# Kernel optimization log

Hardware: AMD Instinct MI355X
Metric: run time of the kernel (lower is better)

Reference implementation:

```python
import jax, jax.numpy as jnp
import numpy as np

D = 2048      # hidden_size
H = 16        # heads
HD = D // H   # head_dim = 128
FF = 8192     # intermediate_size
B = 4
S = 2048
FACTOR = 0.5  # mod_router_factor
EPS = 1e-6


def setup_inputs() -> dict:
    key = jax.random.key(0)
    ks = jax.random.split(key, 10)
    w = lambda k, shape: jax.random.normal(k, shape, jnp.float32) * 0.02
    return {
        "hidden_states": jax.random.normal(ks[0], (B, S, D), jnp.float32),
        "position_ids": jnp.arange(S, dtype=jnp.int32)[None, :],
        "mod_target_mask": jnp.ones((B, S), dtype=bool),
        "attention_mask_2d": jnp.ones((B, S), dtype=bool),
        "router_w": w(ks[1], (D,)),
        "ln1_w": jnp.ones((D,), jnp.float32),
        "ln2_w": jnp.ones((D,), jnp.float32),
        "Wq": w(ks[2], (D, D)),
        "Wk": w(ks[3], (D, D)),
        "Wv": w(ks[4], (D, D)),
        "Wo": w(ks[5], (D, D)),
        "W1": w(ks[6], (D, FF)),
        "W2": w(ks[7], (FF, D)),
    }


def _rmsnorm(x, w):
    return x * jax.lax.rsqrt(jnp.mean(x * x, axis=-1, keepdims=True) + EPS) * w


def _rope(x, pos):
    # x: [B,K,H,HD], pos: [B,K]
    half = HD // 2
    freqs = 1.0 / (10000.0 ** (jnp.arange(half, dtype=jnp.float32) / half))
    ang = pos[:, :, None].astype(jnp.float32) * freqs  # [B,K,half]
    cos = jnp.cos(ang)[:, :, None, :]
    sin = jnp.sin(ang)[:, :, None, :]
    x1, x2 = x[..., :half], x[..., half:]
    return jnp.concatenate([x1 * cos - x2 * sin, x2 * cos + x1 * sin], axis=-1)


def reference(hidden_states, position_ids, mod_target_mask, attention_mask_2d,
              router_w, ln1_w, ln2_w, Wq, Wk, Wv, Wo, W1, W2):
    Bq, Sq, _ = hidden_states.shape
    K = int(Sq * FACTOR)  # static top-k length (all rows fully mod-targeted)

    # --- token router ---
    logits = jnp.einsum('bsd,d->bs', hidden_states, router_w)
    logits = jnp.where(mod_target_mask, logits, -jnp.inf)
    weights = jax.nn.sigmoid(logits)  # weight_normalization: sigmoid * 1.0 + 0.0

    # --- top-k dispatch (indices sorted to preserve sequence order, matching
    # torch boolean-mask gather of kept tokens) ---
    _, idx = jax.lax.top_k(weights, K)
    idx = jnp.sort(idx, axis=1)                       # [B,K]
    bidx = jnp.arange(Bq)[:, None]
    kept = hidden_states[bidx, idx]                   # [B,K,D] residual
    pos = jnp.broadcast_to(position_ids, (Bq, Sq))[bidx, idx]

    # --- decoder layer (Llama-style pre-norm block) on kept tokens ---
    h1 = _rmsnorm(kept, ln1_w)
    q = _rope((h1 @ Wq).reshape(Bq, K, H, HD), pos)
    k = _rope((h1 @ Wk).reshape(Bq, K, H, HD), pos)
    v = (h1 @ Wv).reshape(Bq, K, H, HD)
    scores = jnp.einsum('bqhd,bkhd->bhqk', q, k) / np.sqrt(HD).astype(np.float32)
    causal = jnp.tril(jnp.ones((K, K), dtype=bool))
    scores = jnp.where(causal, scores, jnp.finfo(scores.dtype).min)
    attn = jax.nn.softmax(scores, axis=-1)
    ao = jnp.einsum('bhqk,bkhd->bqhd', attn, v).reshape(Bq, K, D) @ Wo
    h2 = kept + ao
    mlp = jax.nn.gelu(_rmsnorm(h2, ln2_w) @ W1) @ W2
    delta = ao + mlp  # forward_return_residual: layer_out - residual

    # --- combine: hidden[kept]=delta; hidden[target]*=w; hidden[kept]+=residual ---
    out = hidden_states.at[bidx, idx].set(delta)
    out = jnp.where(mod_target_mask[..., None], out * weights[..., None], out)
    out = out.at[bidx, idx].add(kept)
    return out
```

## Files before the change

### kernel.cpp

```cpp
#include <hip/hip_runtime.h>
#include <stdint.h>

#define Dm 2048
#define Hn 16
#define HDm 128
#define FFm 8192
#define Bm 4
#define Sm 2048
#define Km 1024

typedef __attribute__((ext_vector_type(4))) float f32x4;
typedef __attribute__((ext_vector_type(8))) short s16x8;
typedef unsigned short u16;
typedef unsigned int u32;

__device__ __forceinline__ float bf_lo(u32 u){ u32 x = u << 16; return __builtin_bit_cast(float, x); }
__device__ __forceinline__ float bf_hi(u32 u){ u32 x = u & 0xffff0000u; return __builtin_bit_cast(float, x); }
__device__ __forceinline__ float bfu(u16 u){ u32 x = ((u32)u) << 16; return __builtin_bit_cast(float, x); }
__device__ __forceinline__ u16 f2bf(float f){
  u32 u = __builtin_bit_cast(u32, f);
  u += 0x7fffu + ((u >> 16) & 1u);
  return (u16)(u >> 16);
}
__device__ __forceinline__ u32 pack2(float a, float b){
  return (u32)f2bf(a) | ((u32)f2bf(b) << 16);
}
__device__ __forceinline__ void unpack8(uint4 a, float* f){
  f[0]=bf_lo(a.x); f[1]=bf_hi(a.x); f[2]=bf_lo(a.y); f[3]=bf_hi(a.y);
  f[4]=bf_lo(a.z); f[5]=bf_hi(a.z); f[6]=bf_lo(a.w); f[7]=bf_hi(a.w);
}
__device__ __forceinline__ uint4 pack8(const float* f){
  uint4 o; o.x=pack2(f[0],f[1]); o.y=pack2(f[2],f[3]); o.z=pack2(f[4],f[5]); o.w=pack2(f[6],f[7]); return o;
}
__device__ __forceinline__ void load8_in(const void* p, size_t off, int fp32, float* f){
  if (fp32){
    const float* pf = (const float*)p + off;
    float4 a = *(const float4*)pf;
    float4 b = *(const float4*)(pf + 4);
    f[0]=a.x; f[1]=a.y; f[2]=a.z; f[3]=a.w;
    f[4]=b.x; f[5]=b.y; f[6]=b.z; f[7]=b.w;
  } else {
    uint4 a = *(const uint4*)((const u16*)p + off);
    unpack8(a, f);
  }
}
__device__ __forceinline__ float gelu_f(float x){
  float t = tanhf(0.7978845608028654f*(x + 0.044715f*x*x*x));
  return 0.5f*x*(1.0f + t);
}
__device__ __forceinline__ float block_sum256(float s){
  #pragma unroll
  for (int off = 32; off; off >>= 1) s += __shfl_xor(s, off);
  __shared__ float red[4];
  int lane = threadIdx.x & 63, w = threadIdx.x >> 6;
  if (lane == 0) red[w] = s;
  __syncthreads();
  return red[0] + red[1] + red[2] + red[3];
}
__device__ __forceinline__ void gload_lds16(const u16* g, u16* l){
  __builtin_amdgcn_global_load_lds((const __attribute__((address_space(1))) void*)g,
                                   (__attribute__((address_space(3))) void*)l, 16, 0, 0);
}

__global__ __launch_bounds__(256) void sniff_kernel(const u32* __restrict__ hs, int* __restrict__ flag){
  __shared__ int s;
  if (threadIdx.x == 0) s = 0;
  __syncthreads();
  int bad = 0;
  for (int i = threadIdx.x; i < 4096; i += 256){
    u32 w = hs[i];
    float lo = bf_lo(w), hi = bf_hi(w);
    if (!(fabsf(lo) < 1000.f && fabsf(hi) < 1000.f)) bad = 1;
  }
  if (bad) atomicOr(&s, 1);
  __syncthreads();
  if (threadIdx.x == 0) flag[0] = s;
}

__global__ __launch_bounds__(256) void router_kernel(const void* __restrict__ hs, const void* __restrict__ rw,
                                                     const int* __restrict__ dflag,
                                                     float* __restrict__ weights, int* __restrict__ selmap){
  int fp32 = *dflag;
  int row = blockIdx.x, t = threadIdx.x;
  float a[8], b8[8];
  load8_in(hs, (size_t)row*Dm + t*8, fp32, a);
  load8_in(rw, (size_t)t*8, fp32, b8);
  float s = 0.f;
  #pragma unroll
  for (int i = 0; i < 8; i++) s += a[i]*b8[i];
  float tot = block_sum256(s);
  if (t == 0){
    weights[row] = 1.0f/(1.0f + expf(-tot));
    selmap[row] = -1;
  }
}

__global__ __launch_bounds__(1024) void topk_kernel(const float* __restrict__ weights, const int* __restrict__ position_ids,
                                                    int* __restrict__ idx, int* __restrict__ pos, int* __restrict__ selmap){
  int b = blockIdx.x, t = threadIdx.x;
  __shared__ float v[Sm];
  __shared__ int id[Sm];
  v[t] = weights[b*Sm + t];             id[t] = t;
  v[t+1024] = weights[b*Sm + t + 1024]; id[t+1024] = t + 1024;
  for (int size = 2; size <= Sm; size <<= 1){
    for (int stride = size >> 1; stride > 0; stride >>= 1){
      __syncthreads();
      int lo = ((t & ~(stride-1)) << 1) | (t & (stride-1));
      int hi = lo + stride;
      bool up = (lo & size) == 0;
      float va = v[lo], vb = v[hi]; int ia = id[lo], ib = id[hi];
      bool aFirst = (va > vb) || (va == vb && ia < ib);
      if (up ? !aFirst : aFirst){ v[lo]=vb; v[hi]=va; id[lo]=ib; id[hi]=ia; }
    }
  }
  __syncthreads();
  for (int size = 2; size <= Km; size <<= 1){
    for (int stride = size >> 1; stride > 0; stride >>= 1){
      __syncthreads();
      if (t < Km/2){
        int lo = ((t & ~(stride-1)) << 1) | (t & (stride-1));
        int hi = lo + stride;
        bool up = (lo & size) == 0;
        int ia = id[lo], ib = id[hi];
        bool aFirst = ia < ib;
        if (up ? !aFirst : aFirst){ id[lo]=ib; id[hi]=ia; }
      }
    }
  }
  __syncthreads();
  if (t < Km){
    int iv = id[t];
    idx[b*Km + t] = iv;
    pos[b*Km + t] = position_ids[iv];
    selmap[b*Sm + iv] = t;
  }
}

__global__ __launch_bounds__(256) void gather_rmsnorm(const void* __restrict__ hs, const int* __restrict__ idx,
                                                      const void* __restrict__ ln1, const int* __restrict__ dflag,
                                                      u16* __restrict__ h1){
  int fp32 = *dflag;
  int g = blockIdx.x, t = threadIdx.x;
  int b = g >> 10;
  int row = idx[g];
  float f[8];
  load8_in(hs, ((size_t)b*Sm + row)*Dm + t*8, fp32, f);
  float ss = 0.f;
  #pragma unroll
  for (int i = 0; i < 8; i++) ss += f[i]*f[i];
  float tot = block_sum256(ss);
  float scale = rsqrtf(tot * (1.0f/Dm) + 1e-6f);
  float lw[8];
  load8_in(ln1, (size_t)t*8, fp32, lw);
  float o[8];
  #pragma unroll
  for (int i = 0; i < 8; i++) o[i] = f[i]*scale*lw[i];
  ((uint4*)(h1 + (size_t)g*Dm))[t] = pack8(o);
}

__global__ __launch_bounds__(256) void h2norm_kernel(const void* __restrict__ hs, const int* __restrict__ idx,
                                                     const u16* __restrict__ ao, const void* __restrict__ ln2,
                                                     const int* __restrict__ dflag, u16* __restrict__ h2n){
  int fp32 = *dflag;
  int g = blockIdx.x, t = threadIdx.x;
  int b = g >> 10;
  int row = idx[g];
  float ke[8], av[8];
  load8_in(hs, ((size_t)b*Sm + row)*Dm + t*8, fp32, ke);
  unpack8(((const uint4*)(ao + (size_t)g*Dm))[t], av);
  float f[8]; float ss = 0.f;
  #pragma unroll
  for (int i = 0; i < 8; i++){ f[i] = ke[i] + av[i]; ss += f[i]*f[i]; }
  float tot = block_sum256(ss);
  float scale = rsqrtf(tot * (1.0f/Dm) + 1e-6f);
  float lw[8];
  load8_in(ln2, (size_t)t*8, fp32, lw);
  float o[8];
  #pragma unroll
  for (int i = 0; i < 8; i++) o[i] = f[i]*scale*lw[i];
  ((uint4*)(h2n + (size_t)g*Dm))[t] = pack8(o);
}

__global__ __launch_bounds__(256) void transpose_k(const void* __restrict__ src, const int* __restrict__ dflag,
                                                   u16* __restrict__ dst, int R, int C, int ldS, size_t srcOff){
  int fp32 = *dflag;
  __shared__ u16 tile[64][72];
  int c0 = blockIdx.x << 6, r0 = blockIdx.y << 6;
  int t = threadIdx.x;
  int rr = t >> 3, cc = (t & 7) * 8;
  #pragma unroll
  for (int p = 0; p < 2; p++){
    float f[8];
    load8_in(src, srcOff + (size_t)(r0 + rr + p*32) * ldS + c0 + cc, fp32, f);
    u16 tmp[8];
    #pragma unroll
    for (int j = 0; j < 8; j++) tmp[j] = f2bf(f[j]);
    *(uint4*)&tile[rr + p*32][cc] = *(const uint4*)tmp;
  }
  __syncthreads();
  int col = t >> 3, r8 = (t & 7) * 8;
  #pragma unroll
  for (int p = 0; p < 2; p++){
    u16 tmp[8];
    #pragma unroll
    for (int j = 0; j < 8; j++) tmp[j] = tile[r8 + j][col + p*32];
    *(uint4*)(dst + (size_t)(c0 + col + p*32) * R + r0 + r8) = *(const uint4*)tmp;
  }
}

__global__ __launch_bounds__(256) void transpose_v(const u16* __restrict__ src, u16* __restrict__ dst){
  __shared__ u16 tile[64][72];
  int bh = blockIdx.z; int b = bh >> 4, h = bh & 15;
  int key0 = blockIdx.x << 6;
  int d0 = blockIdx.y << 6;
  int t = threadIdx.x;
  int rr = t >> 3, cc = (t & 7) * 8;
  #pragma unroll
  for (int p = 0; p < 2; p++){
    uint4 a = *(const uint4*)(src + ((size_t)(b*Km + key0 + rr + p*32))*Dm + h*HDm + d0 + cc);
    *(uint4*)&tile[rr + p*32][cc] = a;
  }
  __syncthreads();
  int col = t >> 3, r8 = (t & 7) * 8;
  #pragma unroll
  for (int p = 0; p < 2; p++){
    u16 tmp[8];
    #pragma unroll
    for (int j = 0; j < 8; j++) tmp[j] = tile[r8 + j][col + p*32];
    *(uint4*)(dst + ((size_t)bh*HDm + d0 + col + p*32)*Km + key0 + r8) = *(const uint4*)tmp;
  }
}

template<int BN>
__global__ __launch_bounds__(512, 2) void gemm256(const u16* __restrict__ A, const u16* __restrict__ BT,
                                                  u16* __restrict__ Cmat, int Kd, int lda, int ldb, int ldc,
                                                  int do_gelu, int accum){
  extern __shared__ u16 lds[];
  constexpr int WC    = BN / 4;
  constexpr int NREP  = BN / 64;
  constexpr int BTILE = BN * 64;
  constexpr int BROWS = BN / 8;
  constexpr int NSTGB = BN / 64;
  const int t    = threadIdx.x;
  const int lane = t & 63, wid = t >> 6;
  const int wr = wid >> 2, wc = wid & 3;
  const int l16 = lane & 15, quad = lane >> 4;
  const int m0 = blockIdx.x * 256, n0 = blockIdx.y * BN;

  const int lrow = lane >> 3;
  const int csw  = (lane & 7) ^ lrow;
  const u16* gA = A  + (size_t)(m0 + wid*32    + lrow) * lda + csw*8;
  const u16* gB = BT + (size_t)(n0 + wid*BROWS + lrow) * ldb + csw*8;

  f32x4 acc[8][NREP];
  #pragma unroll
  for (int i = 0; i < 8; i++)
    #pragma unroll
    for (int j = 0; j < NREP; j++) acc[i][j] = (f32x4){0.f,0.f,0.f,0.f};

  auto STAGE = [&](int buf, int kt){
    u16* la = lds + buf*16384 + (wid*32)*64;
    #pragma unroll
    for (int s = 0; s < 4; s++)
      gload_lds16(gA + (size_t)(s*8)*lda + kt*64, la + (s*8)*64);
    u16* lb = lds + 32768 + buf*BTILE + (wid*BROWS)*64;
    #pragma unroll
    for (int s = 0; s < NSTGB; s++)
      gload_lds16(gB + (size_t)(s*8)*ldb + kt*64, lb + (s*8)*64);
  };

  const int NT = Kd >> 6;
  STAGE(0, 0);
  for (int kt = 0; kt < NT; kt++){
    const int cur = kt & 1;
    if (kt + 1 < NT){
      STAGE(cur ^ 1, kt + 1);
      if constexpr (BN == 256) asm volatile("s_waitcnt vmcnt(8)" ::: "memory");
      else                     asm volatile("s_waitcnt vmcnt(6)" ::: "memory");
    } else {
      asm volatile("s_waitcnt vmcnt(0)" ::: "memory");
    }
    __builtin_amdgcn_s_barrier();
    __builtin_amdgcn_sched_barrier(0);
    const u16* LA = lds + cur*16384;
    const u16* LB = lds + 32768 + cur*BTILE;
    const int rsw = l16 & 7;
    s16x8 bf[NREP][2];
    #pragma unroll
    for (int ni = 0; ni < NREP; ni++)
      #pragma unroll
      for (int ks = 0; ks < 2; ks++)
        bf[ni][ks] = *(const s16x8*)(LB + (wc*WC + ni*16 + l16)*64 + ((ks*4 + quad) ^ rsw)*8);
    #pragma unroll
    for (int mi = 0; mi < 8; mi++){
      const u16* ar = LA + (wr*128 + mi*16 + l16)*64;
      s16x8 a0 = *(const s16x8*)(ar + ((quad     ^ rsw)*8));
      s16x8 a1 = *(const s16x8*)(ar + (((4+quad) ^ rsw)*8));
      __builtin_amdgcn_s_setprio(1);
      #pragma unroll
      for (int ni = 0; ni < NREP; ni++){
        acc[mi][ni] = __builtin_amdgcn_mfma_f32_16x16x32_bf16(a0, bf[ni][0], acc[mi][ni], 0, 0, 0);
        acc[mi][ni] = __builtin_amdgcn_mfma_f32_16x16x32_bf16(a1, bf[ni][1], acc[mi][ni], 0, 0, 0);
      }
      __builtin_amdgcn_s_setprio(0);
    }
    asm volatile("" ::: "memory");
    __builtin_amdgcn_s_barrier();
    __builtin_amdgcn_sched_barrier(0);
  }

  if (accum){
    __syncthreads();
    float* Cf = (float*)lds;
    #pragma unroll
    for (int mi = 0; mi < 8; mi++)
      #pragma unroll
      for (int ni = 0; ni < NREP; ni++){
        int rb = wr*128 + mi*16 + quad*4;
        int col = wc*WC + ni*16 + l16;
        #pragma unroll
        for (int r = 0; r < 4; r++) Cf[(rb + r)*BN + col] = acc[mi][ni][r];
      }
    __syncthreads();
    constexpr int CH = (256*BN)/4096;
    #pragma unroll
    for (int i = 0; i < CH; i++){
      int off = i*4096 + t*8;
      int row = off / BN, col = off % BN;
      u16* cp = Cmat + (size_t)(m0 + row)*ldc + n0 + col;
      uint4 old = *(const uint4*)cp;
      float f[8]; unpack8(old, f);
      float4 a = *(const float4*)(Cf + off);
      float4 b2 = *(const float4*)(Cf + off + 4);
      float o[8] = {a.x+f[0], a.y+f[1], a.z+f[2], a.w+f[3],
                    b2.x+f[4], b2.y+f[5], b2.z+f[6], b2.w+f[7]};
      *(uint4*)cp = pack8(o);
    }
  } else {
    __syncthreads();
    u16* Ct = lds;
    #pragma unroll
    for (int mi = 0; mi < 8; mi++)
      #pragma unroll
      for (int ni = 0; ni < NREP; ni++){
        int rb = wr*128 + mi*16 + quad*4;
        int col = wc*WC + ni*16 + l16;
        #pragma unroll
        for (int r = 0; r < 4; r++){
          float v = acc[mi][ni][r];
          if (do_gelu) v = gelu_f(v);
          Ct[(rb + r)*BN + col] = f2bf(v);
        }
      }
    __syncthreads();
    constexpr int CH = (256*BN)/4096;
    #pragma unroll
    for (int i = 0; i < CH; i++){
      int off = i*4096 + t*8;
      int row = off / BN, col = off % BN;
      uint4 v = *(const uint4*)(Ct + off);
      *(uint4*)(Cmat + (size_t)(m0 + row)*ldc + n0 + col) = v;
    }
  }
}

__global__ __launch_bounds__(256) void rope_kernel(u16* __restrict__ qkb, const int* __restrict__ pos){
  int tid = blockIdx.x*256 + threadIdx.x;
  int row = tid >> 6, d = tid & 63;
  int grow = row >> 4, h = row & 15;
  float p = (float)pos[grow];
  float freq = exp2f(-0.20762050593589063f * (float)d);
  float ang = p * freq;
  float cs = cosf(ang), sn = sinf(ang);
  size_t base = (size_t)grow * 4096 + h*HDm + d;
  float x1 = bfu(qkb[base]), x2 = bfu(qkb[base+64]);
  qkb[base]    = f2bf(x1*cs - x2*sn);
  qkb[base+64] = f2bf(x2*cs + x1*sn);
  x1 = bfu(qkb[base+2048]); x2 = bfu(qkb[base+2048+64]);
  qkb[base+2048]    = f2bf(x1*cs - x2*sn);
  qkb[base+2048+64] = f2bf(x2*cs + x1*sn);
}

__global__ __launch_bounds__(256) void attn_mfma(const u16* __restrict__ qk, const u16* __restrict__ vt,
                                                 u16* __restrict__ o){
  __shared__ __align__(16) u16 Plds[4][32][72];
  const int w = threadIdx.x >> 6;
  const int lane = threadIdx.x & 63;
  const int l16 = lane & 15, quad = lane >> 4;
  const int bh = blockIdx.y;
  const int b = bh >> 4, h = bh & 15;
  const int bxr = (int)gridDim.x - 1 - (int)blockIdx.x;
  const int q0 = bxr * 128 + w * 32;
  const int QLD = 4096;

  s16x8 aq[2][4];
  #pragma unroll
  for (int qt = 0; qt < 2; qt++){
    const u16* qrow = qk + ((size_t)b*Km + q0 + qt*16 + l16)*QLD + h*HDm;
    #pragma unroll
    for (int kk = 0; kk < 4; kk++) aq[qt][kk] = *(const s16x8*)(qrow + kk*32 + quad*8);
  }
  const u16* kbase = qk + (size_t)b*Km*QLD + 2048 + h*HDm;
  const u16* vth   = vt + (size_t)bh * HDm * Km;

  f32x4 accO[2][8];
  #pragma unroll
  for (int qt = 0; qt < 2; qt++)
    #pragma unroll
    for (int n = 0; n < 8; n++) accO[qt][n] = (f32x4){0.f,0.f,0.f,0.f};
  float mrow[2][4], lrow[2][4];
  #pragma unroll
  for (int qt = 0; qt < 2; qt++)
    #pragma unroll
    for (int r = 0; r < 4; r++){ mrow[qt][r] = -1e30f; lrow[qt][r] = 0.f; }

  const float c = 0.08838834764831845f * 1.4426950408889634f;
  const int qmax = q0 + 31;

  for (int kt = 0; kt <= qmax; kt += 64){
    float sv[4][2][4];
    #pragma unroll
    for (int half = 0; half < 4; half++){
      s16x8 bk[4];
      const u16* krow = kbase + (size_t)(kt + half*16 + l16)*QLD;
      #pragma unroll
      for (int kk = 0; kk < 4; kk++) bk[kk] = *(const s16x8*)(krow + kk*32 + quad*8);
      int key = kt + half*16 + l16;
      #pragma unroll
      for (int qt = 0; qt < 2; qt++){
        f32x4 s = (f32x4){0.f,0.f,0.f,0.f};
        #pragma unroll
        for (int kk = 0; kk < 4; kk++)
          s = __builtin_amdgcn_mfma_f32_16x16x32_bf16(aq[qt][kk], bk[kk], s, 0, 0, 0);
        #pragma unroll
        for (int r = 0; r < 4; r++)
          sv[half][qt][r] = (key <= q0 + qt*16 + quad*4 + r) ? s[r]*c : -1e30f;
      }
    }
    float alpha[2][4];
    #pragma unroll
    for (int qt = 0; qt < 2; qt++){
      #pragma unroll
      for (int r = 0; r < 4; r++){
        float cm = fmaxf(fmaxf(sv[0][qt][r], sv[1][qt][r]), fmaxf(sv[2][qt][r], sv[3][qt][r]));
        cm = fmaxf(cm, __shfl_xor(cm, 1));
        cm = fmaxf(cm, __shfl_xor(cm, 2));
        cm = fmaxf(cm, __shfl_xor(cm, 4));
        cm = fmaxf(cm, __shfl_xor(cm, 8));
        float mn = fmaxf(mrow[qt][r], cm);
        alpha[qt][r] = __builtin_amdgcn_exp2f(mrow[qt][r] - mn);
        mrow[qt][r] = mn;
        float ps = 0.f;
        #pragma unroll
        for (int hh = 0; hh < 4; hh++){
          float p = __builtin_amdgcn_exp2f(sv[hh][qt][r] - mn);
          u16 u = f2bf(p);
          Plds[w][qt*16 + quad*4 + r][hh*16 + l16] = u;
          ps += bfu(u);
        }
        ps += __shfl_xor(ps, 1);
        ps += __shfl_xor(ps, 2);
        ps += __shfl_xor(ps, 4);
        ps += __shfl_xor(ps, 8);
        lrow[qt][r] = lrow[qt][r]*alpha[qt][r] + ps;
      }
    }
    asm volatile("s_waitcnt lgkmcnt(0)" ::: "memory");
    __builtin_amdgcn_sched_barrier(0);
    s16x8 ap[2][2];
    #pragma unroll
    for (int qt = 0; qt < 2; qt++){
      ap[qt][0] = *(const s16x8*)&Plds[w][qt*16 + l16][quad*8];
      ap[qt][1] = *(const s16x8*)&Plds[w][qt*16 + l16][32 + quad*8];
    }
    #pragma unroll
    for (int qt = 0; qt < 2; qt++)
      #pragma unroll
      for (int n = 0; n < 8; n++)
        #pragma unroll
        for (int r = 0; r < 4; r++) accO[qt][n][r] *= alpha[qt][r];
    #pragma unroll
    for (int n = 0; n < 8; n++){
      const u16* vrow = vth + (size_t)(n*16 + l16)*Km + kt;
      s16x8 bv0 = *(const s16x8*)(vrow + quad*8);
      s16x8 bv1 = *(const s16x8*)(vrow + 32 + quad*8);
      accO[0][n] = __builtin_amdgcn_mfma_f32_16x16x32_bf16(ap[0][0], bv0, accO[0][n], 0, 0, 0);
      accO[0][n] = __builtin_amdgcn_mfma_f32_16x16x32_bf16(ap[0][1], bv1, accO[0][n], 0, 0, 0);
      accO[1][n] = __builtin_amdgcn_mfma_f32_16x16x32_bf16(ap[1][0], bv0, accO[1][n], 0, 0, 0);
      accO[1][n] = __builtin_amdgcn_mfma_f32_16x16x32_bf16(ap[1][1], bv1, accO[1][n], 0, 0, 0);
    }
  }

  #pragma unroll
  for (int qt = 0; qt < 2; qt++){
    float inv[4];
    #pragma unroll
    for (int r = 0; r < 4; r++) inv[r] = 1.0f / lrow[qt][r];
    #pragma unroll
    for (int n = 0; n < 8; n++)
      #pragma unroll
      for (int r = 0; r < 4; r++){
        size_t off = ((size_t)b*Km + q0 + qt*16 + quad*4 + r)*Dm + h*HDm + n*16 + l16;
        o[off] = f2bf(accO[qt][n][r]*inv[r]);
      }
  }
}

__global__ __launch_bounds__(256) void final_kernel(const void* __restrict__ hidden, const float* __restrict__ weights,
                                                    const int* __restrict__ selmap, const u16* __restrict__ delta,
                                                    const int* __restrict__ dflag, void* __restrict__ outv){
  int fp32 = *dflag;
  int row = blockIdx.x, t = threadIdx.x;
  int b = row >> 11;
  float w = weights[row];
  int sel = selmap[row];
  float hv[8];
  load8_in(hidden, (size_t)row*Dm + t*8, fp32, hv);
  float f[8];
  if (sel >= 0){
    size_t ko = ((size_t)(b*Km + sel))*Dm;
    float dv[8];
    unpack8(((const uint4*)(delta+ko))[t], dv);
    #pragma unroll
    for (int i = 0; i < 8; i++) f[i] = dv[i]*w + hv[i];
  } else {
    #pragma unroll
    for (int i = 0; i < 8; i++) f[i] = hv[i]*w;
  }
  if (fp32){
    float* o = (float*)outv + (size_t)row*Dm + t*8;
    float4 x; x.x=f[0]; x.y=f[1]; x.z=f[2]; x.w=f[3];
    float4 y; y.x=f[4]; y.y=f[5]; y.z=f[6]; y.w=f[7];
    *(float4*)o = x; *(float4*)(o+4) = y;
  } else {
    ((uint4*)((u16*)outv + (size_t)row*Dm))[t] = pack8(f);
  }
}

extern "C" void kernel_launch(void* const* d_in, const int* in_sizes, int n_in,
                              void* d_out, int out_size, void* d_ws, size_t ws_size,
                              hipStream_t stream){
  (void)in_sizes; (void)n_in; (void)out_size; (void)ws_size;
  const void* hidden      = d_in[0];
  const int* position_ids = (const int*)d_in[1];
  const void* router_w = d_in[4];
  const void* ln1 = d_in[5];
  const void* ln2 = d_in[6];
  const void* Wq  = d_in[7];
  const void* Wk  = d_in[8];
  const void* Wv  = d_in[9];
  const void* Wo  = d_in[10];
  const void* W1  = d_in[11];
  const void* W2  = d_in[12];
  char* ws = (char*)d_ws;
  const size_t MB = 1ull << 20;
  float* weights = (float*)ws;
  int* idx     = (int*)(ws + 32768);
  int* pos     = (int*)(ws + 49152);
  int* selmap  = (int*)(ws + 65536);
  int* dflag   = (int*)(ws + 98304);
  u16* bufB  = (u16*)(ws +  1*MB);
  u16* qkbuf = (u16*)(ws + 17*MB);
  u16* aoB   = qkbuf;
  u16* TWbig = (u16*)(ws + 33*MB);
  u16* TW8   = (u16*)(ws + 49*MB);
  u16* vb   = (u16*)d_out;
  u16* TWqk = (u16*)d_out + 8ull*MB;
  u16* VT   = TWqk;
  u16* gbuf = (u16*)d_out;

  sniff_kernel<<<1, 256, 0, stream>>>((const u32*)hidden, dflag);
  router_kernel<<<Bm*Sm, 256, 0, stream>>>(hidden, router_w, dflag, weights, selmap);
  topk_kernel<<<Bm, 1024, 0, stream>>>(weights, position_ids, idx, pos, selmap);
  gather_rmsnorm<<<Bm*Km, 256, 0, stream>>>(hidden, idx, ln1, dflag, bufB);

  transpose_k<<<dim3(32,32), 256, 0, stream>>>(Wq, dflag, TWqk, Dm, Dm, Dm, 0);
  transpose_k<<<dim3(32,32), 256, 0, stream>>>(Wk, dflag, TWqk + (size_t)2048*2048, Dm, Dm, Dm, 0);
  gemm256<256><<<dim3(16,16), 512, 131072, stream>>>(bufB, TWqk, qkbuf, Dm, Dm, Dm, 4096, 0, 0);
  transpose_k<<<dim3(32,32), 256, 0, stream>>>(Wv, dflag, TW8, Dm, Dm, Dm, 0);
  gemm256<128><<<dim3(16,16), 512, 98304, stream>>>(bufB, TW8, vb, Dm, Dm, Dm, Dm, 0, 0);

  rope_kernel<<<16384, 256, 0, stream>>>(qkbuf, pos);
  transpose_v<<<dim3(16,2,64), 256, 0, stream>>>(vb, VT);
  attn_mfma<<<dim3(8,64), 256, 0, stream>>>(qkbuf, VT, bufB);

  transpose_k<<<dim3(32,32), 256, 0, stream>>>(Wo, dflag, TW8, Dm, Dm, Dm, 0);
  gemm256<128><<<dim3(16,16), 512, 98304, stream>>>(bufB, TW8, aoB, Dm, Dm, Dm, Dm, 0, 0);

  h2norm_kernel<<<Bm*Km, 256, 0, stream>>>(hidden, idx, aoB, ln2, dflag, bufB);

  for (int c = 0; c < 2; c++){
    transpose_k<<<dim3(64,32), 256, 0, stream>>>(W1, dflag, TWbig, Dm, 4096, FFm, (size_t)c*4096);
    gemm256<256><<<dim3(16,16), 512, 131072, stream>>>(bufB, TWbig, gbuf, Dm, Dm, Dm, 4096, 1, 0);
    transpose_k<<<dim3(32,64), 256, 0, stream>>>(W2, dflag, TWbig, 4096, Dm, Dm, (size_t)c*4096*Dm);
    gemm256<128><<<dim3(16,16), 512, 131072, stream>>>(gbuf, TWbig, aoB, 4096, 4096, 4096, Dm, 0, 1);
  }

  final_kernel<<<Bm*Sm, 256, 0, stream>>>(hidden, weights, selmap, aoB, dflag, d_out);
}
```

Before: 961.4 us.

## Fuse QKV weight transposes, swizzle GEMM blocks, prefetch K tiles in attention

Merges the three Q/K/V weight transpose launches into one kernel indexed by blockIdx.z. GEMM block indices are remapped across 8 groups, presumably to spread work across the XCDs for better L2 locality. The attention kernel now prefetches the next 64-key K tile into registers while computing on the current one, and gets a launch-bounds occupancy hint of 2. The extra K registers could raise register pressure, and that pressure works against the occupancy hint.

Result: no change. 967.6 us (+0.6%).

```diff
diff --git a/kernel.cpp b/kernel.cpp
--- a/kernel.cpp
+++ b/kernel.cpp
@@ -208,6 +208,37 @@
   }
 }
 
+__global__ __launch_bounds__(256) void transpose_qkv(const void* __restrict__ Wq, const void* __restrict__ Wk,
+                                                     const void* __restrict__ Wv, const int* __restrict__ dflag,
+                                                     u16* __restrict__ dqk, u16* __restrict__ dv){
+  int fp32 = *dflag;
+  __shared__ u16 tile[64][72];
+  int z = blockIdx.z;
+  const void* src = (z == 0) ? Wq : (z == 1) ? Wk : Wv;
+  u16* dst = (z == 0) ? dqk : (z == 1) ? dqk + (size_t)2048*2048 : dv;
+  int c0 = blockIdx.x << 6, r0 = blockIdx.y << 6;
+  int t = threadIdx.x;
+  int rr = t >> 3, cc = (t & 7) * 8;
+  #pragma unroll
+  for (int p = 0; p < 2; p++){
+    float f[8];
+    load8_in(src, (size_t)(r0 + rr + p*32) * 2048 + c0 + cc, fp32, f);
+    u16 tmp[8];
+    #pragma unroll
+    for (int j = 0; j < 8; j++) tmp[j] = f2bf(f[j]);
+    *(uint4*)&tile[rr + p*32][cc] = *(const uint4*)tmp;
+  }
+  __syncthreads();
+  int col = t >> 3, r8 = (t & 7) * 8;
+  #pragma unroll
+  for (int p = 0; p < 2; p++){
+    u16 tmp[8];
+    #pragma unroll
+    for (int j = 0; j < 8; j++) tmp[j] = tile[r8 + j][col + p*32];
+    *(uint4*)(dst + (size_t)(c0 + col + p*32) * 2048 + r0 + r8) = *(const uint4*)tmp;
+  }
+}
+
 __global__ __launch_bounds__(256) void transpose_v(const u16* __restrict__ src, u16* __restrict__ dst){
   __shared__ u16 tile[64][72];
   int bh = blockIdx.z; int b = bh >> 4, h = bh & 15;
@@ -245,7 +276,11 @@
   const int lane = t & 63, wid = t >> 6;
   const int wr = wid >> 2, wc = wid & 3;
   const int l16 = lane & 15, quad = lane >> 4;
-  const int m0 = blockIdx.x * 256, n0 = blockIdx.y * BN;
+  const int bid0 = (int)(blockIdx.y * gridDim.x + blockIdx.x);
+  const int cpx  = (int)(gridDim.x * gridDim.y) >> 3;
+  const int swz  = (bid0 & 7) * cpx + (bid0 >> 3);
+  const int m0 = (swz % (int)gridDim.x) * 256;
+  const int n0 = (swz / (int)gridDim.x) * BN;
 
   const int lrow = lane >> 3;
   const int csw  = (lane & 7) ^ lrow;
@@ -381,8 +416,8 @@
   qkb[base+2048+64] = f2bf(x2*cs + x1*sn);
 }
 
-__global__ __launch_bounds__(256) void attn_mfma(const u16* __restrict__ qk, const u16* __restrict__ vt,
-                                                 u16* __restrict__ o){
+__global__ __launch_bounds__(256, 2) void attn_mfma(const u16* __restrict__ qk, const u16* __restrict__ vt,
+                                                    u16* __restrict__ o){
   __shared__ __align__(16) u16 Plds[4][32][72];
   const int w = threadIdx.x >> 6;
   const int lane = threadIdx.x & 63;
@@ -417,24 +452,36 @@
   const float c = 0.08838834764831845f * 1.4426950408889634f;
   const int qmax = q0 + 31;
 
+  s16x8 bk[4][4];
+  #pragma unroll
+  for (int half = 0; half < 4; half++){
+    const u16* krow = kbase + (size_t)(half*16 + l16)*QLD;
+    #pragma unroll
+    for (int kk = 0; kk < 4; kk++) bk[half][kk] = *(const s16x8*)(krow + kk*32 + quad*8);
+  }
+
   for (int kt = 0; kt <= qmax; kt += 64){
     float sv[4][2][4];
     #pragma unroll
     for (int half = 0; half < 4; half++){
-      s16x8 bk[4];
-      const u16* krow = kbase + (size_t)(kt + half*16 + l16)*QLD;
-      #pragma unroll
-      for (int kk = 0; kk < 4; kk++) bk[kk] = *(const s16x8*)(krow + kk*32 + quad*8);
       int key = kt + half*16 + l16;
       #pragma unroll
       for (int qt = 0; qt < 2; qt++){
         f32x4 s = (f32x4){0.f,0.f,0.f,0.f};
         #pragma unroll
         for (int kk = 0; kk < 4; kk++)
-          s = __builtin_amdgcn_mfma_f32_16x16x32_bf16(aq[qt][kk], bk[kk], s, 0, 0, 0);
+          s = __builtin_amdgcn_mfma_f32_16x16x32_bf16(aq[qt][kk], bk[half][kk], s, 0, 0, 0);
         #pragma unroll
         for (int r = 0; r < 4; r++)
           sv[half][qt][r] = (key <= q0 + qt*16 + quad*4 + r) ? s[r]*c : -1e30f;
+      }
+    }
+    if (kt + 64 <= qmax){
+      #pragma unroll
+      for (int half = 0; half < 4; half++){
+        const u16* krow = kbase + (size_t)(kt + 64 + half*16 + l16)*QLD;
+        #pragma unroll
+        for (int kk = 0; kk < 4; kk++) bk[half][kk] = *(const s16x8*)(krow + kk*32 + quad*8);
       }
     }
     float alpha[2][4];
@@ -574,10 +621,8 @@
   topk_kernel<<<Bm, 1024, 0, stream>>>(weights, position_ids, idx, pos, selmap);
   gather_rmsnorm<<<Bm*Km, 256, 0, stream>>>(hidden, idx, ln1, dflag, bufB);
 
-  transpose_k<<<dim3(32,32), 256, 0, stream>>>(Wq, dflag, TWqk, Dm, Dm, Dm, 0);
-  transpose_k<<<dim3(32,32), 256, 0, stream>>>(Wk, dflag, TWqk + (size_t)2048*2048, Dm, Dm, Dm, 0);
+  transpose_qkv<<<dim3(32,32,3), 256, 0, stream>>>(Wq, Wk, Wv, dflag, TWqk, TW8);
   gemm256<256><<<dim3(16,16), 512, 131072, stream>>>(bufB, TWqk, qkbuf, Dm, Dm, Dm, 4096, 0, 0);
-  transpose_k<<<dim3(32,32), 256, 0, stream>>>(Wv, dflag, TW8, Dm, Dm, Dm, 0);
   gemm256<128><<<dim3(16,16), 512, 98304, stream>>>(bufB, TW8, vb, Dm, Dm, Dm, Dm, 0, 0);
 
   rope_kernel<<<16384, 256, 0, stream>>>(qkbuf, pos);
```
